# Kernel tuning notes

Measured on AMD Instinct MI355X. Metric: run time of the kernel, lower is better.

Reference implementation:

```python
import jax, jax.numpy as jnp
import numpy as np

TOPK = 9
ALPHA = 0.25
GAMMA = 2.0


def setup_inputs() -> dict:
    key = jax.random.key(0)
    ks = jax.random.split(key, 5)
    B, N, C, G = 16, 21504, 80, 64
    return {
        "pred_logits": jax.random.normal(ks[0], (B, N, C), dtype=jnp.float32),
        "pred_boxes": jax.random.uniform(ks[1], (B, N, 4), dtype=jnp.float32),
        "locations": jax.random.uniform(ks[2], (N, 2), dtype=jnp.float32),
        "gt_boxes": jax.random.uniform(ks[3], (B, G, 4), dtype=jnp.float32),
        "gt_labels": jax.random.randint(ks[4], (B, G), 0, C),
    }


def _cxcywh_to_xyxy(b):
    c, wh = b[..., :2], b[..., 2:]
    return jnp.concatenate([c - 0.5 * wh, c + 0.5 * wh], axis=-1)


def _giou_pairwise(a, b):
    # elementwise GIoU between matched xyxy boxes [..., 4] -> [...]
    area_a = (a[..., 2] - a[..., 0]) * (a[..., 3] - a[..., 1])
    area_b = (b[..., 2] - b[..., 0]) * (b[..., 3] - b[..., 1])
    lt = jnp.maximum(a[..., :2], b[..., :2])
    rb = jnp.minimum(a[..., 2:], b[..., 2:])
    wh = jnp.clip(rb - lt, 0.0)
    inter = wh[..., 0] * wh[..., 1]
    union = area_a + area_b - inter
    iou = inter / union
    lt_c = jnp.minimum(a[..., :2], b[..., :2])
    rb_c = jnp.maximum(a[..., 2:], b[..., 2:])
    wh_c = jnp.clip(rb_c - lt_c, 0.0)
    area_c = wh_c[..., 0] * wh_c[..., 1]
    return iou - (area_c - union) / area_c


def _forward(pred_logits, pred_boxes, locations, gt_boxes, gt_labels):
    B, N, C = pred_logits.shape
    G = gt_boxes.shape[1]
    k = min(TOPK, N)
    # distances from every location to every gt center: [B, G, N]
    centers = gt_boxes[..., :2]
    d = jnp.linalg.norm(centers[:, :, None, :] - locations[None, None, :, :], axis=-1)
    # k nearest locations per gt (ascending distance): idx [B, G, k]
    _, idx = jax.lax.top_k(-d, k)
    b_ix = jnp.arange(B)[:, None, None]
    # scatter one-hot positive labels: target_classes[b, idx, label] = 1
    target_classes = (
        jnp.zeros((B, N, C), pred_logits.dtype)
        .at[b_ix, idx, gt_labels[:, :, None]]
        .set(1.0)
    )
    # sigmoid focal loss, reduction='mean'
    x, t = pred_logits, target_classes
    prob = jax.nn.sigmoid(x)
    ce = -(t * jax.nn.log_sigmoid(x) + (1.0 - t) * jax.nn.log_sigmoid(-x))
    p_t = prob * t + (1.0 - prob) * (1.0 - t)
    focal = (ALPHA * t + (1.0 - ALPHA) * (1.0 - t)) * ce * (1.0 - p_t) ** GAMMA
    loss_cls = focal.mean()
    # per-batch L1 / GIoU over the G*k matched pairs, then mean over batches
    pred = pred_boxes[b_ix, idx]                          # [B, G, k, 4]
    tgt = jnp.broadcast_to(gt_boxes[:, :, None, :], pred.shape)
    loss_bbox = jnp.abs(pred - tgt).mean(axis=(1, 2, 3)).mean()
    giou = _giou_pairwise(_cxcywh_to_xyxy(pred), _cxcywh_to_xyxy(tgt))  # [B, G, k]
    loss_giou = (1.0 - giou).mean(axis=(1, 2)).mean()
    return loss_cls, loss_bbox, loss_giou


def reference(pred_logits, pred_boxes, locations, gt_boxes, gt_labels):
    return _forward(pred_logits, pred_boxes, locations, gt_boxes, gt_labels)
```

## Files before the change

### kernel.cpp

```cpp
#include <hip/hip_runtime.h>
#include <hip/hip_bf16.h>
#include <float.h>

#define BB 16
#define NN 21504
#define CC 80
#define GG 64
#define KK 9
#define NSEG 4
#define SEG4 (NN / 2 / NSEG)
#define T4   (SEG4 / 64)

#define FB 3360
#define FSTRIDE (FB * 256)
#define TOPKB (BB * GG)

__device__ __forceinline__ float focal_t0(float x) {
    float ax = fabsf(x);
    float em = __expf(-ax);
    float sp = __logf(1.0f + em);
    float spx = fmaxf(x, 0.0f) + sp;
    float r = 1.0f / (1.0f + em);
    float p = (x >= 0.0f) ? r : em * r;
    return 0.75f * spx * p * p;
}

__device__ __forceinline__ float focal_corr(float x) {
    float ax = fabsf(x);
    float em = __expf(-ax);
    float sp = __logf(1.0f + em);
    float spx = fmaxf(x, 0.0f) + sp;
    float spn = fmaxf(-x, 0.0f) + sp;
    float r = 1.0f / (1.0f + em);
    float p = (x >= 0.0f) ? r : em * r;
    float q = 1.0f - p;
    float f1 = 0.25f * spn * q * q;
    float f0 = 0.75f * spx * p * p;
    return f1 - f0;
}

__device__ __forceinline__ float d2f(float cx, float cy, float x, float y) {
    float dx = cx - x, dy = cy - y;
    return dx * dx + dy * dy;
}

__global__ __launch_bounds__(256) void k1_seg_focal(
    const float* __restrict__ locations,
    const float* __restrict__ gt_boxes,
    const float* __restrict__ logits,
    float* __restrict__ cand_d,
    int*   __restrict__ cand_n,
    unsigned long long* __restrict__ hdr,
    double* __restrict__ focal_part)
{
    if (blockIdx.x >= TOPKB) {
        int fb = (int)blockIdx.x - TOPKB;
        const float4* v = (const float4*)logits;
        int tid = fb * 256 + threadIdx.x;

        float4 L0 = v[tid + 0 * FSTRIDE];
        float4 L1 = v[tid + 1 * FSTRIDE];
        float4 L2 = v[tid + 2 * FSTRIDE];
        float4 L3 = v[tid + 3 * FSTRIDE];
        float4 L4 = v[tid + 4 * FSTRIDE];
        float4 L5 = v[tid + 5 * FSTRIDE];
        float4 L6 = v[tid + 6 * FSTRIDE];
        float4 L7 = v[tid + 7 * FSTRIDE];

        float s0 = 0.f, s1 = 0.f, s2 = 0.f, s3 = 0.f;
        s0 += focal_t0(L0.x); s1 += focal_t0(L0.y); s2 += focal_t0(L0.z); s3 += focal_t0(L0.w);
        s0 += focal_t0(L1.x); s1 += focal_t0(L1.y); s2 += focal_t0(L1.z); s3 += focal_t0(L1.w);
        s0 += focal_t0(L2.x); s1 += focal_t0(L2.y); s2 += focal_t0(L2.z); s3 += focal_t0(L2.w);
        s0 += focal_t0(L3.x); s1 += focal_t0(L3.y); s2 += focal_t0(L3.z); s3 += focal_t0(L3.w);
        s0 += focal_t0(L4.x); s1 += focal_t0(L4.y); s2 += focal_t0(L4.z); s3 += focal_t0(L4.w);
        s0 += focal_t0(L5.x); s1 += focal_t0(L5.y); s2 += focal_t0(L5.z); s3 += focal_t0(L5.w);
        s0 += focal_t0(L6.x); s1 += focal_t0(L6.y); s2 += focal_t0(L6.z); s3 += focal_t0(L6.w);
        s0 += focal_t0(L7.x); s1 += focal_t0(L7.y); s2 += focal_t0(L7.z); s3 += focal_t0(L7.w);

        double d = (double)((s0 + s1) + (s2 + s3));
#pragma unroll
        for (int o = 32; o > 0; o >>= 1) d += __shfl_down(d, o);
        __shared__ double wsum[4];
        if ((threadIdx.x & 63) == 0) wsum[threadIdx.x >> 6] = d;
        __syncthreads();
        if (threadIdx.x == 0)
            focal_part[fb] = wsum[0] + wsum[1] + wsum[2] + wsum[3];
        return;
    }

    if (blockIdx.x == 0 && threadIdx.x < 8) hdr[threadIdx.x] = 0ull;

    int seg  = threadIdx.x >> 6;
    int lane = threadIdx.x & 63;
    int pair = blockIdx.x;
    int b = pair >> 6;
    int g = pair & (GG - 1);

    const float4 gt = ((const float4*)gt_boxes)[b * GG + g];
    float cx = gt.x, cy = gt.y;
    const float4* loc4 = (const float4*)locations;
    int base4 = seg * SEG4 + lane;

    float m0 = FLT_MAX, m1 = FLT_MAX, m2 = FLT_MAX, m3 = FLT_MAX;
    for (int t = 0; t < T4; t += 7) {
        float4 L0 = loc4[base4 + (t + 0) * 64];
        float4 L1 = loc4[base4 + (t + 1) * 64];
        float4 L2 = loc4[base4 + (t + 2) * 64];
        float4 L3 = loc4[base4 + (t + 3) * 64];
        float4 L4 = loc4[base4 + (t + 4) * 64];
        float4 L5 = loc4[base4 + (t + 5) * 64];
        float4 L6 = loc4[base4 + (t + 6) * 64];
        m0 = fminf(m0, fminf(d2f(cx, cy, L0.x, L0.y), d2f(cx, cy, L0.z, L0.w)));
        m1 = fminf(m1, fminf(d2f(cx, cy, L1.x, L1.y), d2f(cx, cy, L1.z, L1.w)));
        m2 = fminf(m2, fminf(d2f(cx, cy, L2.x, L2.y), d2f(cx, cy, L2.z, L2.w)));
        m3 = fminf(m3, fminf(d2f(cx, cy, L3.x, L3.y), d2f(cx, cy, L3.z, L3.w)));
        m0 = fminf(m0, fminf(d2f(cx, cy, L4.x, L4.y), d2f(cx, cy, L4.z, L4.w)));
        m1 = fminf(m1, fminf(d2f(cx, cy, L5.x, L5.y), d2f(cx, cy, L5.z, L5.w)));
        m2 = fminf(m2, fminf(d2f(cx, cy, L6.x, L6.y), d2f(cx, cy, L6.z, L6.w)));
    }
    float md = fminf(fminf(m0, m1), fminf(m2, m3));

    float v = md;
    float T = FLT_MAX;
    for (int r = 0; r < KK; ++r) {
        float m = v;
        for (int s = 1; s < 64; s <<= 1) m = fminf(m, __shfl_xor(m, s));
        T = m;
        if (v == m) v = FLT_MAX;
    }

    float sd0 = FLT_MAX, sd1 = FLT_MAX, sd2 = FLT_MAX,
          sd3 = FLT_MAX, sd4 = FLT_MAX, sd5 = FLT_MAX;
    int   sn0 = 0x7fffffff, sn1 = 0x7fffffff, sn2 = 0x7fffffff,
          sn3 = 0x7fffffff, sn4 = 0x7fffffff, sn5 = 0x7fffffff;
    int cnt = 0;
#define PUSH(dv, nv)                                             \
    do {                                                         \
        if (cnt == 0)      { sd0 = dv; sn0 = nv; }               \
        else if (cnt == 1) { sd1 = dv; sn1 = nv; }               \
        else if (cnt == 2) { sd2 = dv; sn2 = nv; }               \
        else if (cnt == 3) { sd3 = dv; sn3 = nv; }               \
        else if (cnt == 4) { sd4 = dv; sn4 = nv; }               \
        else if (cnt == 5) { sd5 = dv; sn5 = nv; }               \
        ++cnt;                                                   \
    } while (0)
#define TEST(Lv, tt)                                             \
    do {                                                         \
        int i4 = base4 + (tt) * 64;                              \
        float da = d2f(cx, cy, Lv.x, Lv.y);                      \
        float db = d2f(cx, cy, Lv.z, Lv.w);                      \
        if (da <= T) PUSH(da, 2 * i4);                           \
        if (db <= T) PUSH(db, 2 * i4 + 1);                       \
    } while (0)

    for (int t = 0; t < T4; t += 7) {
        float4 L0 = loc4[base4 + (t + 0) * 64];
        float4 L1 = loc4[base4 + (t + 1) * 64];
        float4 L2 = loc4[base4 + (t + 2) * 64];
        float4 L3 = loc4[base4 + (t + 3) * 64];
        float4 L4 = loc4[base4 + (t + 4) * 64];
        float4 L5 = loc4[base4 + (t + 5) * 64];
        float4 L6 = loc4[base4 + (t + 6) * 64];
        TEST(L0, t + 0);
        TEST(L1, t + 1);
        TEST(L2, t + 2);
        TEST(L3, t + 3);
        TEST(L4, t + 4);
        TEST(L5, t + 5);
        TEST(L6, t + 6);
    }
#undef TEST
#undef PUSH

    int ovf = (cnt > 6) ? 1 : 0;
    for (int s = 1; s < 64; s <<= 1) ovf = max(ovf, __shfl_xor(ovf, s));

    int obase = (pair * NSEG + seg) * KK;
    if (ovf == 0) {
        for (int r = 0; r < KK; ++r) {
            float bv = sd0; int bn = sn0;
            bool c;
            c = sd1 < bv; bv = c ? sd1 : bv; bn = c ? sn1 : bn;
            c = sd2 < bv; bv = c ? sd2 : bv; bn = c ? sn2 : bn;
            c = sd3 < bv; bv = c ? sd3 : bv; bn = c ? sn3 : bn;
            c = sd4 < bv; bv = c ? sd4 : bv; bn = c ? sn4 : bn;
            c = sd5 < bv; bv = c ? sd5 : bv; bn = c ? sn5 : bn;
            for (int s = 1; s < 64; s <<= 1) {
                float ov = __shfl_xor(bv, s);
                int   on = __shfl_xor(bn, s);
                bool cc = (ov < bv) || (ov == bv && on < bn);
                bv = cc ? ov : bv;
                bn = cc ? on : bn;
            }
            if (sn0 == bn) sd0 = FLT_MAX;
            if (sn1 == bn) sd1 = FLT_MAX;
            if (sn2 == bn) sd2 = FLT_MAX;
            if (sn3 == bn) sd3 = FLT_MAX;
            if (sn4 == bn) sd4 = FLT_MAX;
            if (sn5 == bn) sd5 = FLT_MAX;
            if (lane == 0) { cand_d[obase + r] = bv; cand_n[obase + r] = bn; }
        }
    } else {
        float lastD = -1.0f; int lastN = -1;
        for (int r = 0; r < KK; ++r) {
            float bv = FLT_MAX; int bn = 0x7fffffff;
            for (int t = 0; t < T4; ++t) {
                int i4 = base4 + t * 64;
                float4 A = loc4[i4];
                float da = d2f(cx, cy, A.x, A.y);
                float db = d2f(cx, cy, A.z, A.w);
                int na = 2 * i4, nb = 2 * i4 + 1;
                bool ga = (da > lastD) || (da == lastD && na > lastN);
                bool ca = ga && ((da < bv) || (da == bv && na < bn));
                bv = ca ? da : bv; bn = ca ? na : bn;
                bool gb = (db > lastD) || (db == lastD && nb > lastN);
                bool cb = gb && ((db < bv) || (db == bv && nb < bn));
                bv = cb ? db : bv; bn = cb ? nb : bn;
            }
            for (int s = 1; s < 64; s <<= 1) {
                float ov = __shfl_xor(bv, s);
                int   on = __shfl_xor(bn, s);
                bool cc = (ov < bv) || (ov == bv && on < bn);
                bv = cc ? ov : bv;
                bn = cc ? on : bn;
            }
            lastD = bv; lastN = bn;
            if (lane == 0) { cand_d[obase + r] = bv; cand_n[obase + r] = bn; }
        }
    }
}

__global__ __launch_bounds__(256) void topk_merge_kernel(
    const float* __restrict__ pred_boxes,
    const float* __restrict__ gt_boxes,
    const float* __restrict__ cand_d,
    const int*   __restrict__ cand_n,
    int* __restrict__ sel,
    double* __restrict__ merge_l1,
    double* __restrict__ merge_gio)
{
    int wv   = threadIdx.x >> 6;
    int lane = threadIdx.x & 63;
    int pair = blockIdx.x * 4 + wv;
    int b = pair >> 6;
    int g = pair & (GG - 1);

    const float4 gt = ((const float4*)gt_boxes)[b * GG + g];

    float vd = FLT_MAX; int vn = 0x7fffffff;
    if (lane < NSEG * KK) {
        vd = cand_d[pair * NSEG * KK + lane];
        vn = cand_n[pair * NSEG * KK + lane];
    }

    int myn = 0;
    for (int r = 0; r < KK; ++r) {
        float bv = vd; int bn = vn;
        for (int s = 1; s < 64; s <<= 1) {
            float ov = __shfl_xor(bv, s);
            int   on = __shfl_xor(bn, s);
            bool cc = (ov < bv) || (ov == bv && on < bn);
            bv = cc ? ov : bv;
            bn = cc ? on : bn;
        }
        if (vn == bn) vd = FLT_MAX;
        if (lane == r) myn = bn;
        if (lane == 0) sel[pair * KK + r] = bn;
    }
    myn = myn < 0 ? 0 : (myn >= NN ? NN - 1 : myn);

    float l1 = 0.0f, gio = 0.0f;
    if (lane < KK) {
        float4 p = ((const float4*)pred_boxes)[b * NN + myn];
        l1 = fabsf(p.x - gt.x) + fabsf(p.y - gt.y) + fabsf(p.z - gt.z) + fabsf(p.w - gt.w);

        float ax1 = p.x - 0.5f * p.z, ay1 = p.y - 0.5f * p.w;
        float ax2 = p.x + 0.5f * p.z, ay2 = p.y + 0.5f * p.w;
        float bx1 = gt.x - 0.5f * gt.z, by1 = gt.y - 0.5f * gt.w;
        float bx2 = gt.x + 0.5f * gt.z, by2 = gt.y + 0.5f * gt.w;

        float area_a = (ax2 - ax1) * (ay2 - ay1);
        float area_b = (bx2 - bx1) * (by2 - by1);
        float ix1 = fmaxf(ax1, bx1), iy1 = fmaxf(ay1, by1);
        float ix2 = fminf(ax2, bx2), iy2 = fminf(ay2, by2);
        float iw = fmaxf(ix2 - ix1, 0.0f), ih = fmaxf(iy2 - iy1, 0.0f);
        float inter = iw * ih;
        float uni = area_a + area_b - inter;
        float iou = inter / uni;
        float ccx1 = fminf(ax1, bx1), ccy1 = fminf(ay1, by1);
        float ccx2 = fmaxf(ax2, bx2), ccy2 = fmaxf(ay2, by2);
        float cw = fmaxf(ccx2 - ccx1, 0.0f), ch = fmaxf(ccy2 - ccy1, 0.0f);
        float ac = cw * ch;
        float giou = iou - (ac - uni) / ac;
        gio = 1.0f - giou;
    }
    for (int o = 32; o > 0; o >>= 1) {
        l1 += __shfl_down(l1, o);
        gio += __shfl_down(gio, o);
    }
    __shared__ float wl1[4], wg[4];
    if (lane == 0) { wl1[wv] = l1; wg[wv] = gio; }
    __syncthreads();
    if (threadIdx.x == 0) {
        merge_l1[blockIdx.x]  = (double)wl1[0] + (double)wl1[1] + (double)wl1[2] + (double)wl1[3];
        merge_gio[blockIdx.x] = (double)wg[0] + (double)wg[1] + (double)wg[2] + (double)wg[3];
    }
}

#define EPB 144
__global__ __launch_bounds__(256) void correction_kernel(
    const float* __restrict__ logits, const int* __restrict__ sel,
    const int* __restrict__ gt_labels, double* __restrict__ acc,
    int* __restrict__ ticket, float* __restrict__ out,
    const double* __restrict__ focal_part,
    const double* __restrict__ merge_l1,
    const double* __restrict__ merge_gio)
{
    int bq = blockIdx.x;
    int b  = bq >> 2;
    int q  = bq & 3;

    __shared__ int keys[GG * KK];
    for (int e = threadIdx.x; e < GG * KK; e += blockDim.x) {
        int g = e / KK;
        int n = sel[(b * GG + g) * KK + (e - g * KK)];
        keys[e] = n * CC + gt_labels[b * GG + g];
    }
    __syncthreads();

    bool active = (threadIdx.x < EPB);
    int e = q * EPB + (active ? threadIdx.x : 0);
    int k = keys[e];
    k = active ? k : -1;

    int dup = 0;
    for (int e2 = 0; e2 < GG * KK; e2 += 8) {
        int k0 = keys[e2 + 0];
        int k1 = keys[e2 + 1];
        int k2 = keys[e2 + 2];
        int k3 = keys[e2 + 3];
        int k4 = keys[e2 + 4];
        int k5 = keys[e2 + 5];
        int k6 = keys[e2 + 6];
        int k7 = keys[e2 + 7];
        int h = 0;
        h |= (int)(k0 == k) & (int)(e2 + 0 < e);
        h |= (int)(k1 == k) & (int)(e2 + 1 < e);
        h |= (int)(k2 == k) & (int)(e2 + 2 < e);
        h |= (int)(k3 == k) & (int)(e2 + 3 < e);
        h |= (int)(k4 == k) & (int)(e2 + 4 < e);
        h |= (int)(k5 == k) & (int)(e2 + 5 < e);
        h |= (int)(k6 == k) & (int)(e2 + 6 < e);
        h |= (int)(k7 == k) & (int)(e2 + 7 < e);
        dup |= h;
    }

    float corr = 0.0f;
    if (active && dup == 0) {
        corr = focal_corr(logits[(long long)b * NN * CC + k]);
    }

    double d = (double)corr;
    if (threadIdx.x < 53) {
        int fb = bq + (threadIdx.x << 6);
        if (fb < FB) d += focal_part[fb];
    }
#pragma unroll
    for (int o = 32; o > 0; o >>= 1) d += __shfl_down(d, o);
    __shared__ double wsum[4];
    if ((threadIdx.x & 63) == 0) wsum[threadIdx.x >> 6] = d;
    __syncthreads();
    __shared__ int amlast;
    if (threadIdx.x == 0) {
        double s1 = 0.0, s2 = 0.0;
#pragma unroll
        for (int i = 0; i < 4; ++i) {
            s1 += merge_l1[bq * 4 + i];
            s2 += merge_gio[bq * 4 + i];
        }
        atomicAdd(&acc[0], wsum[0] + wsum[1] + wsum[2] + wsum[3]);
        atomicAdd(&acc[1], s1);
        atomicAdd(&acc[2], s2);
        __threadfence();
        int t = atomicAdd(ticket, 1);
        amlast = (t == (int)gridDim.x - 1) ? 1 : 0;
    }
    __syncthreads();
    if (threadIdx.x == 0 && amlast) {
        double a0 = atomicAdd(&acc[0], 0.0);
        double a1 = atomicAdd(&acc[1], 0.0);
        double a2 = atomicAdd(&acc[2], 0.0);
        out[0] = (float)(a0 / (double)((long long)BB * NN * CC));
        out[1] = (float)(a1 / (double)(BB * GG * KK * 4));
        out[2] = (float)(a2 / (double)(BB * GG * KK));
    }
}

extern "C" void kernel_launch(void* const* d_in, const int* in_sizes, int n_in,
                              void* d_out, int out_size, void* d_ws, size_t ws_size,
                              hipStream_t stream) {
    const float* pred_logits = (const float*)d_in[0];
    const float* pred_boxes  = (const float*)d_in[1];
    const float* locations   = (const float*)d_in[2];
    const float* gt_boxes    = (const float*)d_in[3];
    const int*   gt_labels   = (const int*)d_in[4];
    float* out = (float*)d_out;

    unsigned long long* hdr = (unsigned long long*)d_ws;
    double* acc    = (double*)d_ws;
    int*    ticket = (int*)((char*)d_ws + 24);
    int*    sel    = (int*)((char*)d_ws + 64);
    float*  candd  = (float*)((char*)d_ws + 36928);
    int*    candn  = (int*)((char*)d_ws + 184384);
    double* focal_part = (double*)((char*)d_ws + 331840);
    double* merge_l1   = (double*)((char*)d_ws + 358720);
    double* merge_gio  = (double*)((char*)d_ws + 360768);

    k1_seg_focal<<<TOPKB + FB, 256, 0, stream>>>(
        locations, gt_boxes, pred_logits, candd, candn, hdr, focal_part);

    topk_merge_kernel<<<BB * GG / 4, 256, 0, stream>>>(
        pred_boxes, gt_boxes, candd, candn, sel, merge_l1, merge_gio);

    correction_kernel<<<BB * 4, 256, 0, stream>>>(
        pred_logits, sel, gt_labels, acc, ticket, out,
        focal_part, merge_l1, merge_gio);
}
```

Before: 202.8 us.

## Fuse top-k merge and box losses into the segmented search kernel

Each top-k block now writes its per-segment candidates to shared memory and merges them in-block, then computes the L1 and GIoU box losses directly. This removes the separate merge kernel launch and the global candidate round-trip. The focal blocks also drop their shared-memory reduction and barrier, writing one partial per wave instead. The correction kernel now gathers four times as many focal partials plus per-pair box sums with wave shuffles.

```diff
diff --git a/kernel.cpp b/kernel.cpp
--- a/kernel.cpp
+++ b/kernel.cpp
@@ -14,6 +14,7 @@
 #define FB 3360
 #define FSTRIDE (FB * 256)
 #define TOPKB (BB * GG)
+#define FWAVES (FB * 4)
 
 __device__ __forceinline__ float focal_t0(float x) {
     float ax = fabsf(x);
@@ -44,12 +45,14 @@
     return dx * dx + dy * dy;
 }
 
-__global__ __launch_bounds__(256) void k1_seg_focal(
+__global__ __launch_bounds__(256) void k1_all(
     const float* __restrict__ locations,
     const float* __restrict__ gt_boxes,
     const float* __restrict__ logits,
-    float* __restrict__ cand_d,
-    int*   __restrict__ cand_n,
+    const float* __restrict__ pred_boxes,
+    int*   __restrict__ sel,
+    double* __restrict__ merge_l1,
+    double* __restrict__ merge_gio,
     unsigned long long* __restrict__ hdr,
     double* __restrict__ focal_part)
 {
@@ -80,15 +83,15 @@
         double d = (double)((s0 + s1) + (s2 + s3));
 #pragma unroll
         for (int o = 32; o > 0; o >>= 1) d += __shfl_down(d, o);
-        __shared__ double wsum[4];
-        if ((threadIdx.x & 63) == 0) wsum[threadIdx.x >> 6] = d;
-        __syncthreads();
-        if (threadIdx.x == 0)
-            focal_part[fb] = wsum[0] + wsum[1] + wsum[2] + wsum[3];
+        if ((threadIdx.x & 63) == 0)
+            focal_part[fb * 4 + (threadIdx.x >> 6)] = d;
         return;
     }
 
     if (blockIdx.x == 0 && threadIdx.x < 8) hdr[threadIdx.x] = 0ull;
+
+    __shared__ float lds_d[NSEG * KK];
+    __shared__ int   lds_n[NSEG * KK];
 
     int seg  = threadIdx.x >> 6;
     int lane = threadIdx.x & 63;
@@ -175,7 +178,6 @@
     int ovf = (cnt > 6) ? 1 : 0;
     for (int s = 1; s < 64; s <<= 1) ovf = max(ovf, __shfl_xor(ovf, s));
 
-    int obase = (pair * NSEG + seg) * KK;
     if (ovf == 0) {
         for (int r = 0; r < KK; ++r) {
             float bv = sd0; int bn = sn0;
@@ -198,7 +200,7 @@
             if (sn3 == bn) sd3 = FLT_MAX;
             if (sn4 == bn) sd4 = FLT_MAX;
             if (sn5 == bn) sd5 = FLT_MAX;
-            if (lane == 0) { cand_d[obase + r] = bv; cand_n[obase + r] = bn; }
+            if (lane == 0) { lds_d[seg * KK + r] = bv; lds_n[seg * KK + r] = bn; }
         }
     } else {
         float lastD = -1.0f; int lastN = -1;
@@ -225,85 +227,67 @@
                 bn = cc ? on : bn;
             }
             lastD = bv; lastN = bn;
-            if (lane == 0) { cand_d[obase + r] = bv; cand_n[obase + r] = bn; }
-        }
-    }
-}
-
-__global__ __launch_bounds__(256) void topk_merge_kernel(
-    const float* __restrict__ pred_boxes,
-    const float* __restrict__ gt_boxes,
-    const float* __restrict__ cand_d,
-    const int*   __restrict__ cand_n,
-    int* __restrict__ sel,
-    double* __restrict__ merge_l1,
-    double* __restrict__ merge_gio)
-{
-    int wv   = threadIdx.x >> 6;
-    int lane = threadIdx.x & 63;
-    int pair = blockIdx.x * 4 + wv;
-    int b = pair >> 6;
-    int g = pair & (GG - 1);
-
-    const float4 gt = ((const float4*)gt_boxes)[b * GG + g];
-
-    float vd = FLT_MAX; int vn = 0x7fffffff;
-    if (lane < NSEG * KK) {
-        vd = cand_d[pair * NSEG * KK + lane];
-        vn = cand_n[pair * NSEG * KK + lane];
-    }
-
-    int myn = 0;
-    for (int r = 0; r < KK; ++r) {
-        float bv = vd; int bn = vn;
-        for (int s = 1; s < 64; s <<= 1) {
-            float ov = __shfl_xor(bv, s);
-            int   on = __shfl_xor(bn, s);
-            bool cc = (ov < bv) || (ov == bv && on < bn);
-            bv = cc ? ov : bv;
-            bn = cc ? on : bn;
-        }
-        if (vn == bn) vd = FLT_MAX;
-        if (lane == r) myn = bn;
-        if (lane == 0) sel[pair * KK + r] = bn;
-    }
-    myn = myn < 0 ? 0 : (myn >= NN ? NN - 1 : myn);
-
-    float l1 = 0.0f, gio = 0.0f;
-    if (lane < KK) {
-        float4 p = ((const float4*)pred_boxes)[b * NN + myn];
-        l1 = fabsf(p.x - gt.x) + fabsf(p.y - gt.y) + fabsf(p.z - gt.z) + fabsf(p.w - gt.w);
-
-        float ax1 = p.x - 0.5f * p.z, ay1 = p.y - 0.5f * p.w;
-        float ax2 = p.x + 0.5f * p.z, ay2 = p.y + 0.5f * p.w;
-        float bx1 = gt.x - 0.5f * gt.z, by1 = gt.y - 0.5f * gt.w;
-        float bx2 = gt.x + 0.5f * gt.z, by2 = gt.y + 0.5f * gt.w;
-
-        float area_a = (ax2 - ax1) * (ay2 - ay1);
-        float area_b = (bx2 - bx1) * (by2 - by1);
-        float ix1 = fmaxf(ax1, bx1), iy1 = fmaxf(ay1, by1);
-        float ix2 = fminf(ax2, bx2), iy2 = fminf(ay2, by2);
-        float iw = fmaxf(ix2 - ix1, 0.0f), ih = fmaxf(iy2 - iy1, 0.0f);
-        float inter = iw * ih;
-        float uni = area_a + area_b - inter;
-        float iou = inter / uni;
-        float ccx1 = fminf(ax1, bx1), ccy1 = fminf(ay1, by1);
-        float ccx2 = fmaxf(ax2, bx2), ccy2 = fmaxf(ay2, by2);
-        float cw = fmaxf(ccx2 - ccx1, 0.0f), ch = fmaxf(ccy2 - ccy1, 0.0f);
-        float ac = cw * ch;
-        float giou = iou - (ac - uni) / ac;
-        gio = 1.0f - giou;
-    }
-    for (int o = 32; o > 0; o >>= 1) {
-        l1 += __shfl_down(l1, o);
-        gio += __shfl_down(gio, o);
-    }
-    __shared__ float wl1[4], wg[4];
-    if (lane == 0) { wl1[wv] = l1; wg[wv] = gio; }
+            if (lane == 0) { lds_d[seg * KK + r] = bv; lds_n[seg * KK + r] = bn; }
+        }
+    }
+
     __syncthreads();
-    if (threadIdx.x == 0) {
-        merge_l1[blockIdx.x]  = (double)wl1[0] + (double)wl1[1] + (double)wl1[2] + (double)wl1[3];
-        merge_gio[blockIdx.x] = (double)wg[0] + (double)wg[1] + (double)wg[2] + (double)wg[3];
+    if (threadIdx.x < 64) {
+        float vd = FLT_MAX; int vn = 0x7fffffff;
+        if (lane < NSEG * KK) {
+            vd = lds_d[lane];
+            vn = lds_n[lane];
+        }
+
+        int myn = 0;
+        for (int r = 0; r < KK; ++r) {
+            float bv = vd; int bn = vn;
+            for (int s = 1; s < 64; s <<= 1) {
+                float ov = __shfl_xor(bv, s);
+                int   on = __shfl_xor(bn, s);
+                bool cc = (ov < bv) || (ov == bv && on < bn);
+                bv = cc ? ov : bv;
+                bn = cc ? on : bn;
+            }
+            if (vn == bn) vd = FLT_MAX;
+            if (lane == r) myn = bn;
+            if (lane == 0) sel[pair * KK + r] = bn;
+        }
+        myn = myn < 0 ? 0 : (myn >= NN ? NN - 1 : myn);
+
+        float l1 = 0.0f, gio = 0.0f;
+        if (lane < KK) {
+            float4 p = ((const float4*)pred_boxes)[b * NN + myn];
+            l1 = fabsf(p.x - gt.x) + fabsf(p.y - gt.y) + fabsf(p.z - gt.z) + fabsf(p.w - gt.w);
+
+            float ax1 = p.x - 0.5f * p.z, ay1 = p.y - 0.5f * p.w;
+            float ax2 = p.x + 0.5f * p.z, ay2 = p.y + 0.5f * p.w;
+            float bx1 = gt.x - 0.5f * gt.z, by1 = gt.y - 0.5f * gt.w;
+            float bx2 = gt.x + 0.5f * gt.z, by2 = gt.y + 0.5f * gt.w;
+
+            float area_a = (ax2 - ax1) * (ay2 - ay1);
+            float area_b = (bx2 - bx1) * (by2 - by1);
+            float ix1 = fmaxf(ax1, bx1), iy1 = fmaxf(ay1, by1);
+            float ix2 = fminf(ax2, bx2), iy2 = fminf(ay2, by2);
+            float iw = fmaxf(ix2 - ix1, 0.0f), ih = fmaxf(iy2 - iy1, 0.0f);
+            float inter = iw * ih;
+            float uni = area_a + area_b - inter;
+            float iou = inter / uni;
+            float ccx1 = fminf(ax1, bx1), ccy1 = fminf(ay1, by1);
+            float ccx2 = fmaxf(ax2, bx2), ccy2 = fmaxf(ay2, by2);
+            float cw = fmaxf(ccx2 - ccx1, 0.0f), ch = fmaxf(ccy2 - ccy1, 0.0f);
+            float ac = cw * ch;
+            float giou = iou - (ac - uni) / ac;
+            gio = 1.0f - giou;
+        }
+        for (int o = 32; o > 0; o >>= 1) {
+            l1 += __shfl_down(l1, o);
+            gio += __shfl_down(gio, o);
+        }
+        if (lane == 0) {
+            merge_l1[pair]  = (double)l1;
+            merge_gio[pair] = (double)gio;
+        }
     }
 }
 
@@ -319,6 +303,8 @@
     int bq = blockIdx.x;
     int b  = bq >> 2;
     int q  = bq & 3;
+    int wv = threadIdx.x >> 6;
+    int ln = threadIdx.x & 63;
 
     __shared__ int keys[GG * KK];
     for (int e = threadIdx.x; e < GG * KK; e += blockDim.x) {
@@ -361,26 +347,26 @@
     }
 
     double d = (double)corr;
-    if (threadIdx.x < 53) {
-        int fb = bq + (threadIdx.x << 6);
-        if (fb < FB) d += focal_part[fb];
-    }
+    if (threadIdx.x < 210) d += focal_part[bq + (threadIdx.x << 6)];
+
+    double s1 = 0.0, s2 = 0.0;
+    if (wv == 1 && ln < 16) s1 = merge_l1[bq * 16 + ln];
+    if (wv == 2 && ln < 16) s2 = merge_gio[bq * 16 + ln];
+
 #pragma unroll
-    for (int o = 32; o > 0; o >>= 1) d += __shfl_down(d, o);
-    __shared__ double wsum[4];
-    if ((threadIdx.x & 63) == 0) wsum[threadIdx.x >> 6] = d;
+    for (int o = 32; o > 0; o >>= 1) {
+        d  += __shfl_down(d, o);
+        s1 += __shfl_down(s1, o);
+        s2 += __shfl_down(s2, o);
+    }
+    __shared__ double wsum[4], ws1[4], ws2[4];
+    if (ln == 0) { wsum[wv] = d; ws1[wv] = s1; ws2[wv] = s2; }
     __syncthreads();
     __shared__ int amlast;
     if (threadIdx.x == 0) {
-        double s1 = 0.0, s2 = 0.0;
-#pragma unroll
-        for (int i = 0; i < 4; ++i) {
-            s1 += merge_l1[bq * 4 + i];
-            s2 += merge_gio[bq * 4 + i];
-        }
         atomicAdd(&acc[0], wsum[0] + wsum[1] + wsum[2] + wsum[3]);
-        atomicAdd(&acc[1], s1);
-        atomicAdd(&acc[2], s2);
+        atomicAdd(&acc[1], ws1[0] + ws1[1] + ws1[2] + ws1[3]);
+        atomicAdd(&acc[2], ws2[0] + ws2[1] + ws2[2] + ws2[3]);
         __threadfence();
         int t = atomicAdd(ticket, 1);
         amlast = (t == (int)gridDim.x - 1) ? 1 : 0;
@@ -410,17 +396,13 @@
     double* acc    = (double*)d_ws;
     int*    ticket = (int*)((char*)d_ws + 24);
     int*    sel    = (int*)((char*)d_ws + 64);
-    float*  candd  = (float*)((char*)d_ws + 36928);
-    int*    candn  = (int*)((char*)d_ws + 184384);
-    double* focal_part = (double*)((char*)d_ws + 331840);
-    double* merge_l1   = (double*)((char*)d_ws + 358720);
-    double* merge_gio  = (double*)((char*)d_ws + 360768);
-
-    k1_seg_focal<<<TOPKB + FB, 256, 0, stream>>>(
-        locations, gt_boxes, pred_logits, candd, candn, hdr, focal_part);
-
-    topk_merge_kernel<<<BB * GG / 4, 256, 0, stream>>>(
-        pred_boxes, gt_boxes, candd, candn, sel, merge_l1, merge_gio);
+    double* merge_l1   = (double*)((char*)d_ws + 36928);
+    double* merge_gio  = (double*)((char*)d_ws + 45120);
+    double* focal_part = (double*)((char*)d_ws + 53312);
+
+    k1_all<<<TOPKB + FB, 256, 0, stream>>>(
+        locations, gt_boxes, pred_logits, pred_boxes,
+        sel, merge_l1, merge_gio, hdr, focal_part);
 
     correction_kernel<<<BB * 4, 256, 0, stream>>>(
         pred_logits, sel, gt_labels, acc, ticket, out,
```

New measurement: 200.9 us. No clear change (-0.9%).
